# Kernel tuning notes

Hardware: AMD Instinct MI355X
Metric: run time of the kernel (lower is better)

The kernel has to match this reference:

```python
import jax, jax.numpy as jnp
import numpy as np

N, E = 50000, 800000
H, C_IN, C_HID, C_OUT = 4, 256, 64, 64
NEG_SLOPE = 0.2


def leaky_relu(x, s=NEG_SLOPE):
    return jnp.where(x >= 0, x, s * x)


def gat_conv(x, src, dst, W, att_src, att_dst, bias, n_nodes):
    # x: [N, F_in], W: [F_in, H*C], att_*: [1, H, C], bias: [H*C]
    Hh, Cc = att_src.shape[1], att_src.shape[2]
    h = (x @ W).reshape(n_nodes, Hh, Cc)            # [N, H, C]
    a_src = (h * att_src).sum(-1)                   # [N, H]
    a_dst = (h * att_dst).sum(-1)                   # [N, H]
    alpha = leaky_relu(a_src[src] + a_dst[dst])     # [E, H]
    # segment softmax over incoming edges of each destination node
    m = jax.ops.segment_max(alpha, dst, num_segments=n_nodes)   # [N, H]
    e = jnp.exp(alpha - m[dst])                     # [E, H]
    denom = jax.ops.segment_sum(e, dst, num_segments=n_nodes)   # [N, H]
    w = e / jnp.clip(denom, 1e-16)[dst]             # [E, H]
    out = jax.ops.segment_sum(w[:, :, None] * h[src], dst, num_segments=n_nodes)
    return out.reshape(n_nodes, Hh * Cc) + bias


def setup_inputs() -> dict:
    key = jax.random.key(0)
    ks = jax.random.split(key, 10)
    glorot = lambda k, shp: jax.random.normal(k, shp, jnp.float32) * np.sqrt(2.0 / (shp[0] + shp[-1]))
    return {
        "x": jax.random.normal(ks[0], (N, C_IN), jnp.float32),
        "edge_index": jax.random.randint(ks[1], (2, E), 0, N, jnp.int32),
        "W1": glorot(ks[2], (C_IN, H * C_HID)),
        "att_src1": glorot(ks[3], (1, H, C_HID)),
        "att_dst1": glorot(ks[4], (1, H, C_HID)),
        "b1": jnp.zeros((H * C_HID,), jnp.float32),
        "W2": glorot(ks[5], (H * C_HID, H * C_OUT)),
        "att_src2": glorot(ks[6], (1, H, C_OUT)),
        "att_dst2": glorot(ks[7], (1, H, C_OUT)),
        "b2": jnp.zeros((H * C_OUT,), jnp.float32),
    }


def reference(x, edge_index, W1, att_src1, att_dst1, b1, W2, att_src2, att_dst2, b2):
    n = x.shape[0]
    loops = jnp.arange(n, dtype=edge_index.dtype)
    src = jnp.concatenate([edge_index[0], loops])
    dst = jnp.concatenate([edge_index[1], loops])
    h1 = gat_conv(x, src, dst, W1, att_src1, att_dst1, b1, n)
    h1 = jax.nn.relu(h1)
    out = gat_conv(h1, src, dst, W2, att_src2, att_dst2, b2, n)
    return out
```

## Files before the change

### kernel.cpp

```cpp
#include <hip/hip_runtime.h>
#include <math.h>

#define NEG_SLOPE 0.2f

typedef __attribute__((ext_vector_type(8))) short bf16x8;
typedef __attribute__((ext_vector_type(4))) float f32x4;
typedef __attribute__((ext_vector_type(4))) unsigned short u16x4;
typedef __attribute__((ext_vector_type(8))) unsigned short u16x8;

static __device__ __forceinline__ f32x4 lky4(f32x4 v) {
    f32x4 r;
    r.x = v.x >= 0.f ? v.x : NEG_SLOPE * v.x;
    r.y = v.y >= 0.f ? v.y : NEG_SLOPE * v.y;
    r.z = v.z >= 0.f ? v.z : NEG_SLOPE * v.z;
    r.w = v.w >= 0.f ? v.w : NEG_SLOPE * v.w;
    return r;
}
static __device__ __forceinline__ f32x4 exp4(f32x4 v) {
    f32x4 r;
    r.x = __expf(v.x); r.y = __expf(v.y); r.z = __expf(v.z); r.w = __expf(v.w);
    return r;
}
static __device__ __forceinline__ float bf2f(unsigned short u) {
    return __uint_as_float(((unsigned int)u) << 16);
}
static __device__ __forceinline__ unsigned short f2bf_rne(float f) {
    unsigned int u = __float_as_uint(f);
    u += 0x7fffu + ((u >> 16) & 1u);
    return (unsigned short)(u >> 16);
}


__global__ void hist_kernel(const int* __restrict__ dst, int* __restrict__ counts, int E, int Nn) {
    int i = blockIdx.x * blockDim.x + threadIdx.x;
    int tot = E + Nn;
    if (i < tot) {
        int d = (i < E) ? dst[i] : (i - E);
        atomicAdd(&counts[d], 1);
    }
}

__global__ void scan1_kernel(const int* __restrict__ counts, int* __restrict__ partial,
                             int* __restrict__ blockSums, int Nn) {
    __shared__ int sh[1024];
    int b = blockIdx.x, t = threadIdx.x;
    int base = b * 1024;
    int orig[4];
    for (int r = 0; r < 4; r++) {
        int i = t + r * 256;
        int v = (base + i < Nn) ? counts[base + i] : 0;
        orig[r] = v;
        sh[i] = v;
    }
    __syncthreads();
    for (int off = 1; off < 1024; off <<= 1) {
        int vals[4];
        for (int r = 0; r < 4; r++) { int i = t + r * 256; vals[r] = (i >= off) ? sh[i - off] : 0; }
        __syncthreads();
        for (int r = 0; r < 4; r++) { int i = t + r * 256; sh[i] += vals[r]; }
        __syncthreads();
    }
    for (int r = 0; r < 4; r++) {
        int i = t + r * 256;
        if (base + i < Nn) partial[base + i] = sh[i] - orig[r];
    }
    if (t == 0) blockSums[b] = sh[1023];
}

__global__ void scan2_kernel(int* __restrict__ blockSums, int nb) {
    if (threadIdx.x == 0 && blockIdx.x == 0) {
        int s = 0;
        for (int i = 0; i < nb; i++) { int v = blockSums[i]; blockSums[i] = s; s += v; }
    }
}

__global__ void finalize_kernel(const int* __restrict__ partial, const int* __restrict__ blockOff,
                                int* __restrict__ row_ptr, int Nn, int Etot) {
    int i = blockIdx.x * blockDim.x + threadIdx.x;
    if (i < Nn) row_ptr[i] = partial[i] + blockOff[i >> 10];
    if (i == 0) row_ptr[Nn] = Etot;
}

__global__ void scatter_kernel(const int* __restrict__ srcE, const int* __restrict__ dstE,
                               const int* __restrict__ row_ptr, int* __restrict__ fill,
                               int* __restrict__ srcs, int E, int Nn) {
    int i = blockIdx.x * blockDim.x + threadIdx.x;
    int tot = E + Nn;
    if (i < tot) {
        int s, d;
        if (i < E) { s = srcE[i]; d = dstE[i]; }
        else       { s = d = i - E; }
        int pos = row_ptr[d] + atomicAdd(&fill[d], 1);
        srcs[pos] = s;
    }
}

__global__ void convertA_kernel(const float* __restrict__ X, unsigned short* __restrict__ Ab,
                                int rows) {
    int t = blockIdx.x * 256 + threadIdx.x;
    if (t >= rows * 64) return;
    int r = t >> 6, c4 = t & 63;
    f32x4 v = *((const f32x4*)(X + ((size_t)r << 8)) + c4);
    u16x4 o;
    o.x = f2bf_rne(v.x); o.y = f2bf_rne(v.y);
    o.z = f2bf_rne(v.z); o.w = f2bf_rne(v.w);
    *(u16x4*)(Ab + (size_t)r * 256 + c4 * 4) = o;
}

__global__ void transposeW_kernel(const float* __restrict__ W, unsigned short* __restrict__ Bt) {
    int t = blockIdx.x * 256 + threadIdx.x;
    int n = t >> 8, k = t & 255;
    Bt[(size_t)n * 256 + k] = f2bf_rne(W[k * 256 + n]);
}

__global__ __launch_bounds__(256) void gemm_kernel(const unsigned short* __restrict__ Ab,
                                                   const unsigned short* __restrict__ Bt,
                                                   unsigned short* __restrict__ Gb,
                                                   int rows) {
    __shared__ __align__(128) unsigned char smem[65536];

    int tid = threadIdx.x;
    int lane = tid & 63, wid = tid >> 6;
    int wr = wid >> 1, wc = wid & 1;
    int bm = blockIdx.x * 128;
    int bn = blockIdx.y * 128;

    f32x4 zero4 = {0.f, 0.f, 0.f, 0.f};
    f32x4 acc[4][4];
#pragma unroll
    for (int i = 0; i < 4; i++)
#pragma unroll
        for (int j = 0; j < 4; j++) acc[i][j] = zero4;

    int sr = tid >> 3;
    int sc = tid & 7;

    auto stage = [&](int kt, int buf) {
        unsigned short* As = (unsigned short*)(smem + buf * 32768);
        unsigned short* Bs = As + 8192;
#pragma unroll
        for (int q = 0; q < 4; q++) {
            int rt = q * 32 + sr;
            int gr = bm + rt; if (gr >= rows) gr = rows - 1;
            int cg = sc ^ (rt & 7);
            const unsigned short* gp = Ab + (size_t)gr * 256 + kt + cg * 8;
            unsigned short* lp = As + rt * 64 + sc * 8;
            __builtin_amdgcn_global_load_lds(
                (__attribute__((address_space(1))) void*)(uintptr_t)gp,
                (__attribute__((address_space(3))) void*)lp, 16, 0, 0);
        }
#pragma unroll
        for (int q = 0; q < 4; q++) {
            int rt = q * 32 + sr;
            int gn = bn + rt;
            int cg = sc ^ (rt & 7);
            const unsigned short* gp = Bt + (size_t)gn * 256 + kt + cg * 8;
            unsigned short* lp = Bs + rt * 64 + sc * 8;
            __builtin_amdgcn_global_load_lds(
                (__attribute__((address_space(1))) void*)(uintptr_t)gp,
                (__attribute__((address_space(3))) void*)lp, 16, 0, 0);
        }
    };

    stage(0, 0);
    __syncthreads();

    for (int kt = 0; kt < 4; kt++) {
        if (kt < 3) stage((kt + 1) * 64, (kt + 1) & 1);
        unsigned short* As = (unsigned short*)(smem + (kt & 1) * 32768);
        unsigned short* Bs = As + 8192;
#pragma unroll
        for (int ks = 0; ks < 2; ks++) {
            bf16x8 af[4], bfr[4];
#pragma unroll
            for (int f = 0; f < 4; f++) {
                int r = wr * 64 + f * 16 + (lane & 15);
                int c = (ks * 4 + (lane >> 4)) ^ (r & 7);
                af[f] = *(const bf16x8*)(As + r * 64 + c * 8);
                int rb = wc * 64 + f * 16 + (lane & 15);
                int cb = (ks * 4 + (lane >> 4)) ^ (rb & 7);
                bfr[f] = *(const bf16x8*)(Bs + rb * 64 + cb * 8);
            }
#pragma unroll
            for (int i = 0; i < 4; i++)
#pragma unroll
                for (int j = 0; j < 4; j++)
                    acc[i][j] = __builtin_amdgcn_mfma_f32_16x16x32_bf16(af[i], bfr[j], acc[i][j], 0, 0, 0);
        }
        __syncthreads();
    }

    int r0 = wr * 64 + (lane >> 4) * 4;
    int c0 = wc * 64 + (lane & 15);
#pragma unroll
    for (int i = 0; i < 4; i++) {
#pragma unroll
        for (int j = 0; j < 4; j++) {
#pragma unroll
            for (int rg = 0; rg < 4; rg++) {
                int lr = bm + r0 + i * 16 + rg;
                if (lr < rows) {
                    int col = bn + c0 + j * 16;
                    Gb[(size_t)lr * 256 + col] = f2bf_rne(acc[i][j][rg]);
                }
            }
        }
    }
}

__global__ __launch_bounds__(256) void attn_kernel(const unsigned short* __restrict__ Gb,
                                                   const float* __restrict__ att_s,
                                                   const float* __restrict__ att_d,
                                                   float* __restrict__ a_src,
                                                   float* __restrict__ a_dst, int N) {
    int wv = threadIdx.x >> 6, lane = threadIdx.x & 63;
    int n = blockIdx.x * 4 + wv;
    if (n >= N) return;
    u16x4 g4 = *(const u16x4*)(Gb + (size_t)n * 256 + lane * 4);
    f32x4 g;
    g.x = bf2f(g4.x); g.y = bf2f(g4.y); g.z = bf2f(g4.z); g.w = bf2f(g4.w);
    f32x4 s4 = ((const f32x4*)att_s)[lane];
    f32x4 d4 = ((const f32x4*)att_d)[lane];
    f32x4 p = g * s4, q = g * d4;
    float ps = p.x + p.y + p.z + p.w;
    float pd = q.x + q.y + q.z + q.w;
#pragma unroll
    for (int off = 1; off < 16; off <<= 1) {
        ps += __shfl_xor(ps, off);
        pd += __shfl_xor(pd, off);
    }
    if ((lane & 15) == 0) {
        int head = lane >> 4;
        a_src[n * 4 + head] = ps;
        a_dst[n * 4 + head] = pd;
    }
}

__global__ __launch_bounds__(64) void gather_kernel(const unsigned short* __restrict__ Gb,
                                                    const float* __restrict__ a_src,
                                                    const float* __restrict__ a_dst,
                                                    const int* __restrict__ row_ptr,
                                                    const int* __restrict__ srcs,
                                                    const float* __restrict__ bias,
                                                    float* __restrict__ outF,
                                                    unsigned short* __restrict__ outB,
                                                    int N) {
    __shared__ int s_lds[64];
    __shared__ f32x4 w_lds[64];
    int lane = threadIdx.x;
    int n = blockIdx.x;
    if (n >= N) return;
    int half = lane >> 5;
    int sl = lane & 31;
    int head = sl >> 3;

    int start = row_ptr[n], end = row_ptr[n + 1];
    const f32x4* as4p = (const f32x4*)a_src;
    f32x4 adn4 = *(const f32x4*)(a_dst + (size_t)n * 4);

    float acc[8] = {0.f, 0.f, 0.f, 0.f, 0.f, 0.f, 0.f, 0.f};
    f32x4 dsum4 = {0.f, 0.f, 0.f, 0.f};

    for (int c0 = start; c0 < end; c0 += 64) {
        int cnt = min(64, end - c0);
        if (lane < cnt) {
            int s = srcs[c0 + lane];
            f32x4 ev = exp4(lky4(as4p[s] + adn4));
            s_lds[lane] = s;
            w_lds[lane] = ev;
            dsum4 += ev;
        }

        int j = 0;
        for (; j + 7 < cnt; j += 8) {
            int sv_[4]; float wv_[4];
#pragma unroll
            for (int t = 0; t < 4; t++) {
                int e = j + 2 * t + half;
                sv_[t] = s_lds[e];
                wv_[t] = ((const float*)&w_lds[e])[head];
            }
            u16x8 gv_[4];
#pragma unroll
            for (int t = 0; t < 4; t++)
                gv_[t] = *(const u16x8*)(Gb + (size_t)sv_[t] * 256 + sl * 8);
#pragma unroll
            for (int t = 0; t < 4; t++)
#pragma unroll
                for (int k = 0; k < 8; k++)
                    acc[k] = fmaf(bf2f(gv_[t][k]), wv_[t], acc[k]);
        }
        for (; j < cnt; j += 2) {
            int e = j + half;
            if (e < cnt) {
                int s0 = s_lds[e];
                float w0 = ((const float*)&w_lds[e])[head];
                u16x8 g0 = *(const u16x8*)(Gb + (size_t)s0 * 256 + sl * 8);
#pragma unroll
                for (int k = 0; k < 8; k++)
                    acc[k] = fmaf(bf2f(g0[k]), w0, acc[k]);
            }
        }
    }

#pragma unroll
    for (int k = 0; k < 8; k++) acc[k] += __shfl_xor(acc[k], 32);
#pragma unroll
    for (int off = 32; off; off >>= 1) {
        dsum4.x += __shfl_xor(dsum4.x, off);
        dsum4.y += __shfl_xor(dsum4.y, off);
        dsum4.z += __shfl_xor(dsum4.z, off);
        dsum4.w += __shfl_xor(dsum4.w, off);
    }
    float den = head == 0 ? dsum4.x : head == 1 ? dsum4.y : head == 2 ? dsum4.z : dsum4.w;
    float rden = 1.0f / den;

    float r[8];
    const float* bp = bias + sl * 8;
#pragma unroll
    for (int k = 0; k < 8; k++) r[k] = acc[k] * rden + bp[k];

    if (outF) {
        if (half == 0) {
            f32x4 v0 = {r[0], r[1], r[2], r[3]};
            f32x4 v1 = {r[4], r[5], r[6], r[7]};
            f32x4* op = (f32x4*)(outF + (size_t)n * 256 + sl * 8);
            op[0] = v0; op[1] = v1;
        }
    } else {
        if (half == 0) {
            u16x8 v;
#pragma unroll
            for (int k = 0; k < 8; k++) v[k] = f2bf_rne(fmaxf(r[k], 0.f));
            *(u16x8*)(outB + (size_t)n * 256 + sl * 8) = v;
        }
    }
}


extern "C" void kernel_launch(void* const* d_in, const int* in_sizes, int n_in,
                              void* d_out, int out_size, void* d_ws, size_t ws_size,
                              hipStream_t stream) {
    const float* x   = (const float*)d_in[0];
    const int*   ei  = (const int*)d_in[1];
    const float* W1  = (const float*)d_in[2];
    const float* as1 = (const float*)d_in[3];
    const float* ad1 = (const float*)d_in[4];
    const float* b1  = (const float*)d_in[5];
    const float* W2  = (const float*)d_in[6];
    const float* as2 = (const float*)d_in[7];
    const float* ad2 = (const float*)d_in[8];
    const float* b2  = (const float*)d_in[9];

    int N = in_sizes[0] / 256;
    int E = in_sizes[1] / 2;
    int Etot = E + N;
    const int* srcE = ei;
    const int* dstE = ei + E;
    float* out = (float*)d_out;

    char* w = (char*)d_ws;
    size_t used = 0;
    auto alloc = [&](size_t bytes) -> char* {
        char* p = w + used;
        used += (bytes + 255) & ~(size_t)255;
        return p;
    };
    unsigned short* Gb = (unsigned short*)alloc((size_t)N * 256 * 2);
    unsigned short* Ab = (unsigned short*)alloc((size_t)N * 256 * 2);
    float* a_src   = (float*)alloc((size_t)N * 4 * 4);
    float* a_dst   = (float*)alloc((size_t)N * 4 * 4);
    int* counts    = (int*)alloc((size_t)N * 4);
    int* partial   = (int*)alloc((size_t)N * 4);
    int* row_ptr   = (int*)alloc(((size_t)N + 1) * 4);
    int* srcs      = (int*)alloc((size_t)Etot * 4);
    int* blockSums = (int*)alloc(256 * 4);
    unsigned short* Bt = (unsigned short*)alloc((size_t)256 * 256 * 2);

    hipMemsetAsync(counts, 0, (size_t)N * 4, stream);

    hist_kernel<<<(Etot + 255) / 256, 256, 0, stream>>>(dstE, counts, E, N);
    int nScanBlocks = (N + 1023) / 1024;
    scan1_kernel<<<nScanBlocks, 256, 0, stream>>>(counts, partial, blockSums, N);
    scan2_kernel<<<1, 64, 0, stream>>>(blockSums, nScanBlocks);
    finalize_kernel<<<(N + 255) / 256, 256, 0, stream>>>(partial, blockSums, row_ptr, N, Etot);
    hipMemsetAsync(counts, 0, (size_t)N * 4, stream);
    scatter_kernel<<<(Etot + 255) / 256, 256, 0, stream>>>(srcE, dstE, row_ptr, counts, srcs, E, N);

    int nodeBlocks = (N + 3) / 4;
    dim3 gg((N + 127) / 128, 2);

    convertA_kernel<<<(N * 64 + 255) / 256, 256, 0, stream>>>(x, Ab, N);
    transposeW_kernel<<<256, 256, 0, stream>>>(W1, Bt);
    gemm_kernel<<<gg, 256, 0, stream>>>(Ab, Bt, Gb, N);
    attn_kernel<<<nodeBlocks, 256, 0, stream>>>(Gb, as1, ad1, a_src, a_dst, N);
    gather_kernel<<<N, 64, 0, stream>>>(Gb, a_src, a_dst, row_ptr, srcs,
                                        b1, nullptr, Ab, N);

    transposeW_kernel<<<256, 256, 0, stream>>>(W2, Bt);
    gemm_kernel<<<gg, 256, 0, stream>>>(Ab, Bt, Gb, N);
    attn_kernel<<<nodeBlocks, 256, 0, stream>>>(Gb, as2, ad2, a_src, a_dst, N);
    gather_kernel<<<N, 64, 0, stream>>>(Gb, a_src, a_dst, row_ptr, srcs,
                                        b2, out, nullptr, N);
}
```

Measured before the change: 301.9 us.

## Parallelize block-sum scan, fold counts reset into finalize, remap GEMM blocks per XCD

```diff
diff --git a/kernel.cpp b/kernel.cpp
--- a/kernel.cpp
+++ b/kernel.cpp
@@ -68,16 +68,25 @@
 }
 
 __global__ void scan2_kernel(int* __restrict__ blockSums, int nb) {
-    if (threadIdx.x == 0 && blockIdx.x == 0) {
-        int s = 0;
-        for (int i = 0; i < nb; i++) { int v = blockSums[i]; blockSums[i] = s; s += v; }
-    }
+    int lane = threadIdx.x;
+    int v = (lane < nb) ? blockSums[lane] : 0;
+    int orig = v;
+#pragma unroll
+    for (int off = 1; off < 64; off <<= 1) {
+        int u = __shfl_up(v, off);
+        if (lane >= off) v += u;
+    }
+    if (lane < nb) blockSums[lane] = v - orig;
 }
 
 __global__ void finalize_kernel(const int* __restrict__ partial, const int* __restrict__ blockOff,
-                                int* __restrict__ row_ptr, int Nn, int Etot) {
+                                int* __restrict__ row_ptr, int* __restrict__ counts,
+                                int Nn, int Etot) {
     int i = blockIdx.x * blockDim.x + threadIdx.x;
-    if (i < Nn) row_ptr[i] = partial[i] + blockOff[i >> 10];
+    if (i < Nn) {
+        row_ptr[i] = partial[i] + blockOff[i >> 10];
+        counts[i] = 0;
+    }
     if (i == 0) row_ptr[Nn] = Etot;
 }
 
@@ -116,14 +125,19 @@
 __global__ __launch_bounds__(256) void gemm_kernel(const unsigned short* __restrict__ Ab,
                                                    const unsigned short* __restrict__ Bt,
                                                    unsigned short* __restrict__ Gb,
-                                                   int rows) {
+                                                   int rows, int nwg) {
+    int orig = blockIdx.x;
+    int q = nwg >> 3, r8 = nwg & 7;
+    int xcd = orig & 7, idx = orig >> 3;
+    int logical = (xcd < r8 ? xcd * (q + 1) : r8 * (q + 1) + (xcd - r8) * q) + idx;
+    int bm = (logical >> 1) * 128;
+    int bn = (logical & 1) * 128;
+
     __shared__ __align__(128) unsigned char smem[65536];
 
     int tid = threadIdx.x;
     int lane = tid & 63, wid = tid >> 6;
     int wr = wid >> 1, wc = wid & 1;
-    int bm = blockIdx.x * 128;
-    int bn = blockIdx.y * 128;
 
     f32x4 zero4 = {0.f, 0.f, 0.f, 0.f};
     f32x4 acc[4][4];
@@ -139,8 +153,8 @@
         unsigned short* As = (unsigned short*)(smem + buf * 32768);
         unsigned short* Bs = As + 8192;
 #pragma unroll
-        for (int q = 0; q < 4; q++) {
-            int rt = q * 32 + sr;
+        for (int q2 = 0; q2 < 4; q2++) {
+            int rt = q2 * 32 + sr;
             int gr = bm + rt; if (gr >= rows) gr = rows - 1;
             int cg = sc ^ (rt & 7);
             const unsigned short* gp = Ab + (size_t)gr * 256 + kt + cg * 8;
@@ -150,8 +164,8 @@
                 (__attribute__((address_space(3))) void*)lp, 16, 0, 0);
         }
 #pragma unroll
-        for (int q = 0; q < 4; q++) {
-            int rt = q * 32 + sr;
+        for (int q2 = 0; q2 < 4; q2++) {
+            int rt = q2 * 32 + sr;
             int gn = bn + rt;
             int cg = sc ^ (rt & 7);
             const unsigned short* gp = Bt + (size_t)gn * 256 + kt + cg * 8;
@@ -383,22 +397,21 @@
     int nScanBlocks = (N + 1023) / 1024;
     scan1_kernel<<<nScanBlocks, 256, 0, stream>>>(counts, partial, blockSums, N);
     scan2_kernel<<<1, 64, 0, stream>>>(blockSums, nScanBlocks);
-    finalize_kernel<<<(N + 255) / 256, 256, 0, stream>>>(partial, blockSums, row_ptr, N, Etot);
-    hipMemsetAsync(counts, 0, (size_t)N * 4, stream);
+    finalize_kernel<<<(N + 255) / 256, 256, 0, stream>>>(partial, blockSums, row_ptr, counts, N, Etot);
     scatter_kernel<<<(Etot + 255) / 256, 256, 0, stream>>>(srcE, dstE, row_ptr, counts, srcs, E, N);
 
     int nodeBlocks = (N + 3) / 4;
-    dim3 gg((N + 127) / 128, 2);
+    int nwg = ((N + 127) / 128) * 2;
 
     convertA_kernel<<<(N * 64 + 255) / 256, 256, 0, stream>>>(x, Ab, N);
     transposeW_kernel<<<256, 256, 0, stream>>>(W1, Bt);
-    gemm_kernel<<<gg, 256, 0, stream>>>(Ab, Bt, Gb, N);
+    gemm_kernel<<<nwg, 256, 0, stream>>>(Ab, Bt, Gb, N, nwg);
     attn_kernel<<<nodeBlocks, 256, 0, stream>>>(Gb, as1, ad1, a_src, a_dst, N);
     gather_kernel<<<N, 64, 0, stream>>>(Gb, a_src, a_dst, row_ptr, srcs,
                                         b1, nullptr, Ab, N);
 
     transposeW_kernel<<<256, 256, 0, stream>>>(W2, Bt);
-    gemm_kernel<<<gg, 256, 0, stream>>>(Ab, Bt, Gb, N);
+    gemm_kernel<<<nwg, 256, 0, stream>>>(Ab, Bt, Gb, N, nwg);
     attn_kernel<<<nodeBlocks, 256, 0, stream>>>(Gb, as2, ad2, a_src, a_dst, N);
     gather_kernel<<<N, 64, 0, stream>>>(Gb, a_src, a_dst, row_ptr, srcs,
                                         b2, out, nullptr, N);
```

After: 298.1 us. About the same (-1.3%).
